# Optimization experiments

Hardware: AMD Instinct MI355X
Metric: run time of the kernel (lower is better)

## Reference

```python
import jax, jax.numpy as jnp
import numpy as np

# PlatonicConv (graph mode, attention=True, use_key=True): tetrahedron group G=12
G = 12
H_EFF = 2          # num_heads // G = 24 // 12
HEAD_D = 16        # embed_dim_g // H_EFF = (384//12) // 2
GH = G * H_EFF     # 24
IN_C = 384
EMB = 384
OUT_C = 384
N_GRAPHS = 32
NODES_PER_GRAPH = 64
N = N_GRAPHS * NODES_PER_GRAPH   # 2048
SPATIAL = 3


def _fc_edges():
    # fully-connected edges within each graph (batch[src]==batch[dst]), incl. self loops
    n = NODES_PER_GRAPH
    offs = np.arange(N_GRAPHS, dtype=np.int32) * n
    gs, gd = np.meshgrid(np.arange(n, dtype=np.int32), np.arange(n, dtype=np.int32), indexing='ij')
    src = (offs[:, None] + gs.reshape(-1)[None, :]).reshape(-1)
    dst = (offs[:, None] + gd.reshape(-1)[None, :]).reshape(-1)
    return jnp.asarray(src), jnp.asarray(dst)


def setup_inputs() -> dict:
    key = jax.random.key(0)
    ks = jax.random.split(key, 12)
    sw = 1.0 / np.sqrt(IN_C)
    x = jax.random.normal(ks[0], (N, IN_C), jnp.float32)
    pos = jax.random.normal(ks[1], (N, SPATIAL), jnp.float32)
    Wq = jax.random.normal(ks[2], (IN_C, EMB), jnp.float32) * sw
    bq = jnp.zeros((EMB,), jnp.float32)
    Wk = jax.random.normal(ks[3], (IN_C, EMB), jnp.float32) * sw
    bk = jnp.zeros((EMB,), jnp.float32)
    Wv = jax.random.normal(ks[4], (IN_C, EMB), jnp.float32) * sw
    bv = jnp.zeros((EMB,), jnp.float32)
    Wo = jax.random.normal(ks[5], (EMB, OUT_C), jnp.float32) * (1.0 / np.sqrt(EMB))
    bo = jnp.zeros((OUT_C,), jnp.float32)
    # RoPE frequencies: freq_sigma=1.0, random init, per spatial dim / head / half-dim
    rope_freqs = jax.random.normal(ks[6], (SPATIAL, H_EFF, HEAD_D // 2), jnp.float32)
    src, dst = _fc_edges()
    return {"x": x, "pos": pos, "Wq": Wq, "bq": bq, "Wk": Wk, "bk": bk,
            "Wv": Wv, "bv": bv, "Wo": Wo, "bo": bo, "rope_freqs": rope_freqs,
            "src": src, "dst": dst}


def _rope(t, pos, freqs):
    # t: [N, G, H, D]; pos: [N, 3]; freqs: [3, H, D//2]
    theta = jnp.einsum('ns,shf->nhf', pos, freqs)            # [N, H, D/2]
    cos = jnp.cos(theta)[:, None, :, :]                      # broadcast over G
    sin = jnp.sin(theta)[:, None, :, :]
    tr = t.reshape(t.shape[:-1] + (HEAD_D // 2, 2))
    t1, t2 = tr[..., 0], tr[..., 1]
    rot = jnp.stack([t1 * cos - t2 * sin, t1 * sin + t2 * cos], axis=-1)
    return rot.reshape(t.shape)


def reference(x, pos, Wq, bq, Wk, bk, Wv, bv, Wo, bo, rope_freqs, src, dst):
    n = x.shape[0]
    q = (x @ Wq + bq).reshape(n, G, H_EFF, HEAD_D)
    k = (x @ Wk + bk).reshape(n, G, H_EFF, HEAD_D)
    v = (x @ Wv + bv).reshape(n, G, H_EFF, HEAD_D)
    q = _rope(q, pos, rope_freqs)
    k = _rope(k, pos, rope_freqs)
    qf = q.reshape(n, GH, HEAD_D)
    kf = k.reshape(n, GH, HEAD_D)
    vf = v.reshape(n, GH, HEAD_D)
    # gather by edge index
    q_src = qf[src]                                          # [E, GH, D]
    k_dst = kf[dst]
    v_dst = vf[dst]
    scores = jnp.sum(q_src * k_dst, axis=-1) * (HEAD_D ** -0.5)  # [E, GH]
    # scatter softmax over edges grouped by src node (per group-head)
    m = jax.ops.segment_max(scores, src, num_segments=n)     # [N, GH]
    ex = jnp.exp(scores - m[src])
    den = jax.ops.segment_sum(ex, src, num_segments=n)
    a = ex / den[src]                                        # [E, GH]
    out = jax.ops.segment_sum(a[..., None] * v_dst, src, num_segments=n)  # [N, GH, D]
    out = out.reshape(n, GH * HEAD_D)
    return out @ Wo + bo
```

## Files before the change

kernel.cpp:

```cpp
#include <hip/hip_runtime.h>


#define NNODES   2048
#define KDIM     384
#define QKV_N    1152
#define NGRAPHS  32
#define NPG      64
#define GHEADS   24
#define HDIM     16

typedef __attribute__((ext_vector_type(8))) short short8;
typedef __attribute__((ext_vector_type(4))) float f32x4;

__device__ __forceinline__ short f2bf(float f) {
    unsigned u = __builtin_bit_cast(unsigned, f);
    u += 0x7FFFu + ((u >> 16) & 1u);
    return (short)(u >> 16);
}

__global__ __launch_bounds__(256) void prep_kernel(
    const float* __restrict__ x,
    const float* __restrict__ Wq, const float* __restrict__ Wk,
    const float* __restrict__ Wv, const float* __restrict__ Wo,
    const float* __restrict__ bq, const float* __restrict__ bk,
    const float* __restrict__ bv,
    short* __restrict__ WT, short* __restrict__ xb,
    float* __restrict__ bias_cat)
{
    const int b   = blockIdx.x;
    const int tid = threadIdx.x;
    if (b < 576) {
        __shared__ float tile[32][33];
        const int mat = b / 144;
        const int t   = b - mat * 144;
        const int k0  = (t / 12) * 32;
        const int n0  = (t % 12) * 32;
        const float* W = (mat == 0) ? Wq : (mat == 1) ? Wk : (mat == 2) ? Wv : Wo;
        const int cx = tid & 31;
        const int ty = tid >> 5;
        #pragma unroll
        for (int i = 0; i < 4; ++i) {
            const int rr = ty + 8 * i;
            tile[rr][cx] = W[(size_t)(k0 + rr) * KDIM + n0 + cx];
        }
        __syncthreads();
        #pragma unroll
        for (int i = 0; i < 4; ++i) {
            const int rr = ty + 8 * i;
            WT[(size_t)(mat * 384 + n0 + rr) * KDIM + k0 + cx] = f2bf(tile[cx][rr]);
        }
    } else if (b < 960) {
        const int idx = ((b - 576) * 256 + tid) * 8;
        const f32x4* xp = reinterpret_cast<const f32x4*>(x + idx);
        f32x4 v0 = xp[0], v1 = xp[1];
        short8 o;
        o[0] = f2bf(v0[0]); o[1] = f2bf(v0[1]); o[2] = f2bf(v0[2]); o[3] = f2bf(v0[3]);
        o[4] = f2bf(v1[0]); o[5] = f2bf(v1[1]); o[6] = f2bf(v1[2]); o[7] = f2bf(v1[3]);
        *reinterpret_cast<short8*>(xb + idx) = o;
    } else {
        for (int i = tid; i < QKV_N; i += 256) {
            const int seg = i / 384;
            const float* bp = (seg == 0) ? bq : (seg == 1) ? bk : bv;
            bias_cat[i] = bp[i - seg * 384];
        }
    }
}

__global__ __launch_bounds__(256) void gemm_kernel(
    const short* __restrict__ A,
    const short* __restrict__ BT,
    const float* __restrict__ bias,
    float* __restrict__ C, int ldc,
    const float* __restrict__ pos, const float* __restrict__ freqs,
    int do_rope)
{
    __shared__ __align__(16) short As[64 * 72];
    __shared__ __align__(16) short Bs[64 * 72];

    const int tid = threadIdx.x;
    const int m0  = blockIdx.x * 64;
    const int n0  = blockIdx.y * 64;

    const int r  = tid >> 2;
    const int kq = (tid & 3) * 16;

    const int lane = tid & 63;
    const int w    = tid >> 6;
    const int wr   = (w >> 1) * 32;
    const int wc   = (w & 1) * 32;
    const int fr   = lane & 15;
    const int ko   = (lane >> 4) * 8;

    const short* aRow = A  + (size_t)(m0 + r) * KDIM;
    const short* bRow = BT + (size_t)(n0 + r) * KDIM;

    short8 a0 = *reinterpret_cast<const short8*>(aRow + kq);
    short8 a1 = *reinterpret_cast<const short8*>(aRow + kq + 8);
    short8 b0 = *reinterpret_cast<const short8*>(bRow + kq);
    short8 b1 = *reinterpret_cast<const short8*>(bRow + kq + 8);
    *reinterpret_cast<short8*>(&As[r * 72 + kq])     = a0;
    *reinterpret_cast<short8*>(&As[r * 72 + kq + 8]) = a1;
    *reinterpret_cast<short8*>(&Bs[r * 72 + kq])     = b0;
    *reinterpret_cast<short8*>(&Bs[r * 72 + kq + 8]) = b1;
    __syncthreads();

    f32x4 acc[2][2];
    #pragma unroll
    for (int i = 0; i < 2; ++i)
        #pragma unroll
        for (int j = 0; j < 2; ++j)
            acc[i][j] = (f32x4){0.f, 0.f, 0.f, 0.f};

    for (int kt = 0;; kt += 64) {
        const bool has_next = (kt + 64) < KDIM;
        short8 na0, na1, nb0, nb1;
        if (has_next) {
            na0 = *reinterpret_cast<const short8*>(aRow + kt + 64 + kq);
            na1 = *reinterpret_cast<const short8*>(aRow + kt + 64 + kq + 8);
            nb0 = *reinterpret_cast<const short8*>(bRow + kt + 64 + kq);
            nb1 = *reinterpret_cast<const short8*>(bRow + kt + 64 + kq + 8);
        }
        #pragma unroll
        for (int kk = 0; kk < 64; kk += 32) {
            short8 af0 = *reinterpret_cast<const short8*>(&As[(wr + fr) * 72 + kk + ko]);
            short8 af1 = *reinterpret_cast<const short8*>(&As[(wr + 16 + fr) * 72 + kk + ko]);
            short8 bf0 = *reinterpret_cast<const short8*>(&Bs[(wc + fr) * 72 + kk + ko]);
            short8 bf1 = *reinterpret_cast<const short8*>(&Bs[(wc + 16 + fr) * 72 + kk + ko]);
            acc[0][0] = __builtin_amdgcn_mfma_f32_16x16x32_bf16(af0, bf0, acc[0][0], 0, 0, 0);
            acc[0][1] = __builtin_amdgcn_mfma_f32_16x16x32_bf16(af0, bf1, acc[0][1], 0, 0, 0);
            acc[1][0] = __builtin_amdgcn_mfma_f32_16x16x32_bf16(af1, bf0, acc[1][0], 0, 0, 0);
            acc[1][1] = __builtin_amdgcn_mfma_f32_16x16x32_bf16(af1, bf1, acc[1][1], 0, 0, 0);
        }
        if (!has_next) break;
        __syncthreads();
        *reinterpret_cast<short8*>(&As[r * 72 + kq])     = na0;
        *reinterpret_cast<short8*>(&As[r * 72 + kq + 8]) = na1;
        *reinterpret_cast<short8*>(&Bs[r * 72 + kq])     = nb0;
        *reinterpret_cast<short8*>(&Bs[r * 72 + kq + 8]) = nb1;
        __syncthreads();
    }

    const bool rope_wave = do_rope && (n0 < 768);
    #pragma unroll
    for (int ni = 0; ni < 2; ++ni) {
        const int c  = n0 + wc + ni * 16 + fr;
        const float bv = bias[c];
        float F0 = 0.f, F1 = 0.f, F2 = 0.f;
        if (rope_wave) {
            const int f = fr >> 1;
            const int h = (c >> 4) & 1;
            F0 = freqs[h * 8 + f];
            F1 = freqs[16 + h * 8 + f];
            F2 = freqs[32 + h * 8 + f];
        }
        #pragma unroll
        for (int mi = 0; mi < 2; ++mi) {
            const int rowb = m0 + wr + mi * 16 + (lane >> 4) * 4;
            float v[4];
            #pragma unroll
            for (int rr = 0; rr < 4; ++rr)
                v[rr] = acc[mi][ni][rr] + bv;
            if (rope_wave) {
                #pragma unroll
                for (int rr = 0; rr < 4; ++rr) {
                    const int row = rowb + rr;
                    const float th = pos[row * 3] * F0 + pos[row * 3 + 1] * F1
                                   + pos[row * 3 + 2] * F2;
                    const float cs = __cosf(th);
                    const float sn = __sinf(th);
                    const float other = __shfl_xor(v[rr], 1, 64);
                    v[rr] = (fr & 1) ? (other * sn + v[rr] * cs)
                                     : (v[rr] * cs - other * sn);
                }
            }
            #pragma unroll
            for (int rr = 0; rr < 4; ++rr)
                C[(size_t)(rowb + rr) * ldc + c] = v[rr];
        }
    }
}

__global__ __launch_bounds__(64) void attn_kernel(
    const float* __restrict__ qkv,
    short* __restrict__ attn_out)
{
    const int blk  = blockIdx.x;
    const int gr   = blk / GHEADS;
    const int gh   = blk - gr * GHEADS;
    const int lane = threadIdx.x;
    const int n    = gr * NPG + lane;

    const float* rowq = qkv + (size_t)n * QKV_N + gh * HDIM;

    __shared__ float klds[NPG][HDIM];
    __shared__ float vlds[NPG][HDIM];

    f32x4 q[4];
    #pragma unroll
    for (int i = 0; i < 4; ++i)
        q[i] = reinterpret_cast<const f32x4*>(rowq)[i];
    #pragma unroll
    for (int i = 0; i < 4; ++i)
        reinterpret_cast<f32x4*>(&klds[lane][0])[i] =
            reinterpret_cast<const f32x4*>(rowq + 384)[i];
    #pragma unroll
    for (int i = 0; i < 4; ++i)
        reinterpret_cast<f32x4*>(&vlds[lane][0])[i] =
            reinterpret_cast<const f32x4*>(rowq + 768)[i];
    __syncthreads();

    float sc[NPG];
    #pragma unroll
    for (int j = 0; j < NPG; ++j) {
        const f32x4* kp = reinterpret_cast<const f32x4*>(&klds[j][0]);
        f32x4 k0 = kp[0], k1 = kp[1], k2 = kp[2], k3 = kp[3];
        float a = q[0][0]*k0[0] + q[0][1]*k0[1] + q[0][2]*k0[2] + q[0][3]*k0[3]
                + q[1][0]*k1[0] + q[1][1]*k1[1] + q[1][2]*k1[2] + q[1][3]*k1[3]
                + q[2][0]*k2[0] + q[2][1]*k2[1] + q[2][2]*k2[2] + q[2][3]*k2[3]
                + q[3][0]*k3[0] + q[3][1]*k3[1] + q[3][2]*k3[2] + q[3][3]*k3[3];
        sc[j] = a * 0.25f;
    }

    float m = sc[0];
    #pragma unroll
    for (int j = 1; j < NPG; ++j) m = fmaxf(m, sc[j]);

    float den = 0.f;
    #pragma unroll
    for (int j = 0; j < NPG; ++j) {
        sc[j] = __expf(sc[j] - m);
        den += sc[j];
    }

    float o[HDIM];
    #pragma unroll
    for (int d = 0; d < HDIM; ++d) o[d] = 0.f;
    #pragma unroll
    for (int j = 0; j < NPG; ++j) {
        const float p = sc[j];
        const f32x4* vp = reinterpret_cast<const f32x4*>(&vlds[j][0]);
        f32x4 v0 = vp[0], v1 = vp[1], v2 = vp[2], v3 = vp[3];
        #pragma unroll
        for (int d = 0; d < 4; ++d) {
            o[d]      += p * v0[d];
            o[4 + d]  += p * v1[d];
            o[8 + d]  += p * v2[d];
            o[12 + d] += p * v3[d];
        }
    }

    const float inv = 1.0f / den;
    short8 r0, r1;
    #pragma unroll
    for (int d = 0; d < 8; ++d) {
        r0[d] = f2bf(o[d] * inv);
        r1[d] = f2bf(o[8 + d] * inv);
    }
    short* outp = attn_out + (size_t)n * 384 + gh * HDIM;
    *reinterpret_cast<short8*>(outp)     = r0;
    *reinterpret_cast<short8*>(outp + 8) = r1;
}

extern "C" void kernel_launch(void* const* d_in, const int* in_sizes, int n_in,
                              void* d_out, int out_size, void* d_ws, size_t ws_size,
                              hipStream_t stream) {
    const float* x    = (const float*)d_in[0];
    const float* pos  = (const float*)d_in[1];
    const float* Wq   = (const float*)d_in[2];
    const float* bq   = (const float*)d_in[3];
    const float* Wk   = (const float*)d_in[4];
    const float* bk   = (const float*)d_in[5];
    const float* Wv   = (const float*)d_in[6];
    const float* bv   = (const float*)d_in[7];
    const float* Wo   = (const float*)d_in[8];
    const float* bo   = (const float*)d_in[9];
    const float* rope = (const float*)d_in[10];

    char* ws = (char*)d_ws;
    short* WT       = (short*)(ws);
    short* xb       = (short*)(ws + 1179648);
    float* bias_cat = (float*)(ws + 2752512);
    float* qkv      = (float*)(ws + 2757120);
    short* attn     = (short*)(ws + 12194304);

    prep_kernel<<<961, 256, 0, stream>>>(x, Wq, Wk, Wv, Wo, bq, bk, bv,
                                         WT, xb, bias_cat);

    {
        dim3 grid(NNODES / 64, QKV_N / 64);
        gemm_kernel<<<grid, 256, 0, stream>>>(xb, WT, bias_cat, qkv, QKV_N,
                                              pos, rope, 1);
    }

    attn_kernel<<<NGRAPHS * GHEADS, 64, 0, stream>>>(qkv, attn);

    {
        dim3 grid(NNODES / 64, KDIM / 64);
        gemm_kernel<<<grid, 256, 0, stream>>>(attn, WT + (size_t)1152 * KDIM, bo,
                                              (float*)d_out, KDIM, pos, rope, 0);
    }
}
```

Before: 109.8 us.

## Fuse QKV projection with per-graph attention and shrink output GEMM tiles

Each attention block (one graph, one group-head) now computes its own Q, K, V slices with MFMA straight from global bf16 data, applies bias and RoPE, and runs softmax-attention with four waves that split the keys and combine results with cross-lane shuffles. This removes the fp32 QKV round trip through global memory and one kernel launch. The output GEMM becomes a one-wave 16x64 tile kernel with no LDS staging, which gives many more blocks. The trade-off is that tiles are no longer shared through LDS, so the x and weight rows are reloaded from global or L2 by each block.

New measurement: 113.8 us. 1.04x slower.

```diff
diff --git a/kernel.cpp b/kernel.cpp
--- a/kernel.cpp
+++ b/kernel.cpp
@@ -3,7 +3,6 @@
 
 #define NNODES   2048
 #define KDIM     384
-#define QKV_N    1152
 #define NGRAPHS  32
 #define NPG      64
 #define GHEADS   24
@@ -22,10 +21,7 @@
     const float* __restrict__ x,
     const float* __restrict__ Wq, const float* __restrict__ Wk,
     const float* __restrict__ Wv, const float* __restrict__ Wo,
-    const float* __restrict__ bq, const float* __restrict__ bk,
-    const float* __restrict__ bv,
-    short* __restrict__ WT, short* __restrict__ xb,
-    float* __restrict__ bias_cat)
+    short* __restrict__ WT, short* __restrict__ xb)
 {
     const int b   = blockIdx.x;
     const int tid = threadIdx.x;
@@ -49,7 +45,7 @@
             const int rr = ty + 8 * i;
             WT[(size_t)(mat * 384 + n0 + rr) * KDIM + k0 + cx] = f2bf(tile[cx][rr]);
         }
-    } else if (b < 960) {
+    } else {
         const int idx = ((b - 576) * 256 + tid) * 8;
         const f32x4* xp = reinterpret_cast<const f32x4*>(x + idx);
         f32x4 v0 = xp[0], v1 = xp[1];
@@ -57,189 +53,128 @@
         o[0] = f2bf(v0[0]); o[1] = f2bf(v0[1]); o[2] = f2bf(v0[2]); o[3] = f2bf(v0[3]);
         o[4] = f2bf(v1[0]); o[5] = f2bf(v1[1]); o[6] = f2bf(v1[2]); o[7] = f2bf(v1[3]);
         *reinterpret_cast<short8*>(xb + idx) = o;
-    } else {
-        for (int i = tid; i < QKV_N; i += 256) {
-            const int seg = i / 384;
-            const float* bp = (seg == 0) ? bq : (seg == 1) ? bk : bv;
-            bias_cat[i] = bp[i - seg * 384];
-        }
-    }
-}
-
-__global__ __launch_bounds__(256) void gemm_kernel(
-    const short* __restrict__ A,
-    const short* __restrict__ BT,
-    const float* __restrict__ bias,
-    float* __restrict__ C, int ldc,
+    }
+}
+
+__global__ __launch_bounds__(256) void qkv_attn_kernel(
+    const short* __restrict__ xb,
+    const short* __restrict__ WT,
+    const float* __restrict__ bq, const float* __restrict__ bk,
+    const float* __restrict__ bv,
     const float* __restrict__ pos, const float* __restrict__ freqs,
-    int do_rope)
-{
-    __shared__ __align__(16) short As[64 * 72];
-    __shared__ __align__(16) short Bs[64 * 72];
-
-    const int tid = threadIdx.x;
-    const int m0  = blockIdx.x * 64;
-    const int n0  = blockIdx.y * 64;
-
-    const int r  = tid >> 2;
-    const int kq = (tid & 3) * 16;
-
-    const int lane = tid & 63;
-    const int w    = tid >> 6;
-    const int wr   = (w >> 1) * 32;
-    const int wc   = (w & 1) * 32;
-    const int fr   = lane & 15;
-    const int ko   = (lane >> 4) * 8;
-
-    const short* aRow = A  + (size_t)(m0 + r) * KDIM;
-    const short* bRow = BT + (size_t)(n0 + r) * KDIM;
-
-    short8 a0 = *reinterpret_cast<const short8*>(aRow + kq);
-    short8 a1 = *reinterpret_cast<const short8*>(aRow + kq + 8);
-    short8 b0 = *reinterpret_cast<const short8*>(bRow + kq);
-    short8 b1 = *reinterpret_cast<const short8*>(bRow + kq + 8);
-    *reinterpret_cast<short8*>(&As[r * 72 + kq])     = a0;
-    *reinterpret_cast<short8*>(&As[r * 72 + kq + 8]) = a1;
-    *reinterpret_cast<short8*>(&Bs[r * 72 + kq])     = b0;
-    *reinterpret_cast<short8*>(&Bs[r * 72 + kq + 8]) = b1;
-    __syncthreads();
-
-    f32x4 acc[2][2];
-    #pragma unroll
-    for (int i = 0; i < 2; ++i)
-        #pragma unroll
-        for (int j = 0; j < 2; ++j)
-            acc[i][j] = (f32x4){0.f, 0.f, 0.f, 0.f};
-
-    for (int kt = 0;; kt += 64) {
-        const bool has_next = (kt + 64) < KDIM;
-        short8 na0, na1, nb0, nb1;
-        if (has_next) {
-            na0 = *reinterpret_cast<const short8*>(aRow + kt + 64 + kq);
-            na1 = *reinterpret_cast<const short8*>(aRow + kt + 64 + kq + 8);
-            nb0 = *reinterpret_cast<const short8*>(bRow + kt + 64 + kq);
-            nb1 = *reinterpret_cast<const short8*>(bRow + kt + 64 + kq + 8);
-        }
-        #pragma unroll
-        for (int kk = 0; kk < 64; kk += 32) {
-            short8 af0 = *reinterpret_cast<const short8*>(&As[(wr + fr) * 72 + kk + ko]);
-            short8 af1 = *reinterpret_cast<const short8*>(&As[(wr + 16 + fr) * 72 + kk + ko]);
-            short8 bf0 = *reinterpret_cast<const short8*>(&Bs[(wc + fr) * 72 + kk + ko]);
-            short8 bf1 = *reinterpret_cast<const short8*>(&Bs[(wc + 16 + fr) * 72 + kk + ko]);
-            acc[0][0] = __builtin_amdgcn_mfma_f32_16x16x32_bf16(af0, bf0, acc[0][0], 0, 0, 0);
-            acc[0][1] = __builtin_amdgcn_mfma_f32_16x16x32_bf16(af0, bf1, acc[0][1], 0, 0, 0);
-            acc[1][0] = __builtin_amdgcn_mfma_f32_16x16x32_bf16(af1, bf0, acc[1][0], 0, 0, 0);
-            acc[1][1] = __builtin_amdgcn_mfma_f32_16x16x32_bf16(af1, bf1, acc[1][1], 0, 0, 0);
-        }
-        if (!has_next) break;
-        __syncthreads();
-        *reinterpret_cast<short8*>(&As[r * 72 + kq])     = na0;
-        *reinterpret_cast<short8*>(&As[r * 72 + kq + 8]) = na1;
-        *reinterpret_cast<short8*>(&Bs[r * 72 + kq])     = nb0;
-        *reinterpret_cast<short8*>(&Bs[r * 72 + kq + 8]) = nb1;
-        __syncthreads();
-    }
-
-    const bool rope_wave = do_rope && (n0 < 768);
-    #pragma unroll
-    for (int ni = 0; ni < 2; ++ni) {
-        const int c  = n0 + wc + ni * 16 + fr;
-        const float bv = bias[c];
-        float F0 = 0.f, F1 = 0.f, F2 = 0.f;
-        if (rope_wave) {
-            const int f = fr >> 1;
-            const int h = (c >> 4) & 1;
-            F0 = freqs[h * 8 + f];
-            F1 = freqs[16 + h * 8 + f];
-            F2 = freqs[32 + h * 8 + f];
-        }
-        #pragma unroll
-        for (int mi = 0; mi < 2; ++mi) {
-            const int rowb = m0 + wr + mi * 16 + (lane >> 4) * 4;
-            float v[4];
-            #pragma unroll
-            for (int rr = 0; rr < 4; ++rr)
-                v[rr] = acc[mi][ni][rr] + bv;
-            if (rope_wave) {
-                #pragma unroll
-                for (int rr = 0; rr < 4; ++rr) {
-                    const int row = rowb + rr;
-                    const float th = pos[row * 3] * F0 + pos[row * 3 + 1] * F1
-                                   + pos[row * 3 + 2] * F2;
-                    const float cs = __cosf(th);
-                    const float sn = __sinf(th);
-                    const float other = __shfl_xor(v[rr], 1, 64);
-                    v[rr] = (fr & 1) ? (other * sn + v[rr] * cs)
-                                     : (v[rr] * cs - other * sn);
-                }
-            }
-            #pragma unroll
-            for (int rr = 0; rr < 4; ++rr)
-                C[(size_t)(rowb + rr) * ldc + c] = v[rr];
-        }
-    }
-}
-
-__global__ __launch_bounds__(64) void attn_kernel(
-    const float* __restrict__ qkv,
     short* __restrict__ attn_out)
 {
     const int blk  = blockIdx.x;
     const int gr   = blk / GHEADS;
     const int gh   = blk - gr * GHEADS;
-    const int lane = threadIdx.x;
-    const int n    = gr * NPG + lane;
-
-    const float* rowq = qkv + (size_t)n * QKV_N + gh * HDIM;
-
-    __shared__ float klds[NPG][HDIM];
-    __shared__ float vlds[NPG][HDIM];
-
-    f32x4 q[4];
-    #pragma unroll
-    for (int i = 0; i < 4; ++i)
-        q[i] = reinterpret_cast<const f32x4*>(rowq)[i];
-    #pragma unroll
-    for (int i = 0; i < 4; ++i)
-        reinterpret_cast<f32x4*>(&klds[lane][0])[i] =
-            reinterpret_cast<const f32x4*>(rowq + 384)[i];
-    #pragma unroll
-    for (int i = 0; i < 4; ++i)
-        reinterpret_cast<f32x4*>(&vlds[lane][0])[i] =
-            reinterpret_cast<const f32x4*>(rowq + 768)[i];
+    const int tid  = threadIdx.x;
+    const int w    = tid >> 6;
+    const int lane = tid & 63;
+    const int fr   = lane & 15;
+    const int hi   = lane >> 4;
+
+    const short* aP  = xb + (size_t)(gr * 64 + w * 16 + fr) * KDIM + hi * 8;
+    const short* bqP = WT + (size_t)(gh * 16 + fr) * KDIM + hi * 8;
+    const short* bkP = bqP + (size_t)384 * KDIM;
+    const short* bvP = bkP + (size_t)384 * KDIM;
+
+    f32x4 acc[3];
+    acc[0] = (f32x4){0.f, 0.f, 0.f, 0.f};
+    acc[1] = acc[0];
+    acc[2] = acc[0];
+
+    #pragma unroll 4
+    for (int kt = 0; kt < KDIM; kt += 32) {
+        short8 af = *reinterpret_cast<const short8*>(aP + kt);
+        short8 b0 = *reinterpret_cast<const short8*>(bqP + kt);
+        short8 b1 = *reinterpret_cast<const short8*>(bkP + kt);
+        short8 b2 = *reinterpret_cast<const short8*>(bvP + kt);
+        acc[0] = __builtin_amdgcn_mfma_f32_16x16x32_bf16(af, b0, acc[0], 0, 0, 0);
+        acc[1] = __builtin_amdgcn_mfma_f32_16x16x32_bf16(af, b1, acc[1], 0, 0, 0);
+        acc[2] = __builtin_amdgcn_mfma_f32_16x16x32_bf16(af, b2, acc[2], 0, 0, 0);
+    }
+
+    __shared__ float q_lds[64][20];
+    __shared__ float k_lds[64][20];
+    __shared__ float v_lds[64][20];
+
+    const float bias_q = bq[gh * 16 + fr];
+    const float bias_k = bk[gh * 16 + fr];
+    const float bias_v = bv[gh * 16 + fr];
+    const int   h = gh & 1;
+    const int   f = fr >> 1;
+    const float F0 = freqs[h * 8 + f];
+    const float F1 = freqs[16 + h * 8 + f];
+    const float F2 = freqs[32 + h * 8 + f];
+
+    #pragma unroll
+    for (int rr = 0; rr < 4; ++rr) {
+        const int row  = w * 16 + hi * 4 + rr;
+        const int grow = gr * 64 + row;
+        float qv = acc[0][rr] + bias_q;
+        float kv = acc[1][rr] + bias_k;
+        float vv = acc[2][rr] + bias_v;
+        const float th = pos[grow * 3] * F0 + pos[grow * 3 + 1] * F1
+                       + pos[grow * 3 + 2] * F2;
+        const float cs = __cosf(th);
+        const float sn = __sinf(th);
+        const float qo = __shfl_xor(qv, 1, 64);
+        const float ko = __shfl_xor(kv, 1, 64);
+        qv = (fr & 1) ? (qo * sn + qv * cs) : (qv * cs - qo * sn);
+        kv = (fr & 1) ? (ko * sn + kv * cs) : (kv * cs - ko * sn);
+        q_lds[row][fr] = qv;
+        k_lds[row][fr] = kv;
+        v_lds[row][fr] = vv;
+    }
     __syncthreads();
 
-    float sc[NPG];
-    #pragma unroll
-    for (int j = 0; j < NPG; ++j) {
-        const f32x4* kp = reinterpret_cast<const f32x4*>(&klds[j][0]);
-        f32x4 k0 = kp[0], k1 = kp[1], k2 = kp[2], k3 = kp[3];
-        float a = q[0][0]*k0[0] + q[0][1]*k0[1] + q[0][2]*k0[2] + q[0][3]*k0[3]
-                + q[1][0]*k1[0] + q[1][1]*k1[1] + q[1][2]*k1[2] + q[1][3]*k1[3]
-                + q[2][0]*k2[0] + q[2][1]*k2[1] + q[2][2]*k2[2] + q[2][3]*k2[3]
-                + q[3][0]*k3[0] + q[3][1]*k3[1] + q[3][2]*k3[2] + q[3][3]*k3[3];
+    const int qrow = w * 16 + fr;
+    f32x4 q0 = *reinterpret_cast<const f32x4*>(&q_lds[qrow][0]);
+    f32x4 q1 = *reinterpret_cast<const f32x4*>(&q_lds[qrow][4]);
+    f32x4 q2 = *reinterpret_cast<const f32x4*>(&q_lds[qrow][8]);
+    f32x4 q3 = *reinterpret_cast<const f32x4*>(&q_lds[qrow][12]);
+
+    float sc[16];
+    #pragma unroll
+    for (int j = 0; j < 16; ++j) {
+        const float* kp = &k_lds[hi * 16 + j][0];
+        f32x4 k0 = reinterpret_cast<const f32x4*>(kp)[0];
+        f32x4 k1 = reinterpret_cast<const f32x4*>(kp)[1];
+        f32x4 k2 = reinterpret_cast<const f32x4*>(kp)[2];
+        f32x4 k3 = reinterpret_cast<const f32x4*>(kp)[3];
+        float a = q0[0]*k0[0] + q0[1]*k0[1] + q0[2]*k0[2] + q0[3]*k0[3]
+                + q1[0]*k1[0] + q1[1]*k1[1] + q1[2]*k1[2] + q1[3]*k1[3]
+                + q2[0]*k2[0] + q2[1]*k2[1] + q2[2]*k2[2] + q2[3]*k2[3]
+                + q3[0]*k3[0] + q3[1]*k3[1] + q3[2]*k3[2] + q3[3]*k3[3];
         sc[j] = a * 0.25f;
     }
 
-    float m = sc[0];
-    #pragma unroll
-    for (int j = 1; j < NPG; ++j) m = fmaxf(m, sc[j]);
+    float mx = sc[0];
+    #pragma unroll
+    for (int j = 1; j < 16; ++j) mx = fmaxf(mx, sc[j]);
+    mx = fmaxf(mx, __shfl_xor(mx, 16, 64));
+    mx = fmaxf(mx, __shfl_xor(mx, 32, 64));
 
     float den = 0.f;
     #pragma unroll
-    for (int j = 0; j < NPG; ++j) {
-        sc[j] = __expf(sc[j] - m);
+    for (int j = 0; j < 16; ++j) {
+        sc[j] = __expf(sc[j] - mx);
         den += sc[j];
     }
-
-    float o[HDIM];
-    #pragma unroll
-    for (int d = 0; d < HDIM; ++d) o[d] = 0.f;
-    #pragma unroll
-    for (int j = 0; j < NPG; ++j) {
+    den += __shfl_xor(den, 16, 64);
+    den += __shfl_xor(den, 32, 64);
+
+    float o[16];
+    #pragma unroll
+    for (int d = 0; d < 16; ++d) o[d] = 0.f;
+    #pragma unroll
+    for (int j = 0; j < 16; ++j) {
         const float p = sc[j];
-        const f32x4* vp = reinterpret_cast<const f32x4*>(&vlds[j][0]);
-        f32x4 v0 = vp[0], v1 = vp[1], v2 = vp[2], v3 = vp[3];
+        const float* vp = &v_lds[hi * 16 + j][0];
+        f32x4 v0 = reinterpret_cast<const f32x4*>(vp)[0];
+        f32x4 v1 = reinterpret_cast<const f32x4*>(vp)[1];
+        f32x4 v2 = reinterpret_cast<const f32x4*>(vp)[2];
+        f32x4 v3 = reinterpret_cast<const f32x4*>(vp)[3];
         #pragma unroll
         for (int d = 0; d < 4; ++d) {
             o[d]      += p * v0[d];
@@ -248,17 +183,70 @@
             o[12 + d] += p * v3[d];
         }
     }
-
-    const float inv = 1.0f / den;
-    short8 r0, r1;
-    #pragma unroll
-    for (int d = 0; d < 8; ++d) {
-        r0[d] = f2bf(o[d] * inv);
-        r1[d] = f2bf(o[8 + d] * inv);
-    }
-    short* outp = attn_out + (size_t)n * 384 + gh * HDIM;
-    *reinterpret_cast<short8*>(outp)     = r0;
-    *reinterpret_cast<short8*>(outp + 8) = r1;
+    #pragma unroll
+    for (int d = 0; d < 16; ++d) {
+        o[d] += __shfl_xor(o[d], 16, 64);
+        o[d] += __shfl_xor(o[d], 32, 64);
+    }
+
+    if (hi == 0) {
+        const float inv = 1.0f / den;
+        short8 r0, r1;
+        #pragma unroll
+        for (int d = 0; d < 8; ++d) {
+            r0[d] = f2bf(o[d] * inv);
+            r1[d] = f2bf(o[8 + d] * inv);
+        }
+        short* op = attn_out + (size_t)(gr * 64 + qrow) * KDIM + gh * 16;
+        *reinterpret_cast<short8*>(op)     = r0;
+        *reinterpret_cast<short8*>(op + 8) = r1;
+    }
+}
+
+__global__ __launch_bounds__(64) void out_gemm_kernel(
+    const short* __restrict__ A,
+    const short* __restrict__ BT,
+    const float* __restrict__ bias,
+    float* __restrict__ C)
+{
+    const int r0   = blockIdx.x * 16;
+    const int c0   = blockIdx.y * 64;
+    const int lane = threadIdx.x;
+    const int fr   = lane & 15;
+    const int hi   = lane >> 4;
+
+    const short* aP = A + (size_t)(r0 + fr) * KDIM + hi * 8;
+    const short* b0P = BT + (size_t)(c0 + fr) * KDIM + hi * 8;
+    const short* b1P = b0P + (size_t)16 * KDIM;
+    const short* b2P = b1P + (size_t)16 * KDIM;
+    const short* b3P = b2P + (size_t)16 * KDIM;
+
+    f32x4 acc[4];
+    acc[0] = (f32x4){0.f, 0.f, 0.f, 0.f};
+    acc[1] = acc[0]; acc[2] = acc[0]; acc[3] = acc[0];
+
+    #pragma unroll 4
+    for (int kt = 0; kt < KDIM; kt += 32) {
+        short8 af = *reinterpret_cast<const short8*>(aP + kt);
+        short8 f0 = *reinterpret_cast<const short8*>(b0P + kt);
+        short8 f1 = *reinterpret_cast<const short8*>(b1P + kt);
+        short8 f2 = *reinterpret_cast<const short8*>(b2P + kt);
+        short8 f3 = *reinterpret_cast<const short8*>(b3P + kt);
+        acc[0] = __builtin_amdgcn_mfma_f32_16x16x32_bf16(af, f0, acc[0], 0, 0, 0);
+        acc[1] = __builtin_amdgcn_mfma_f32_16x16x32_bf16(af, f1, acc[1], 0, 0, 0);
+        acc[2] = __builtin_amdgcn_mfma_f32_16x16x32_bf16(af, f2, acc[2], 0, 0, 0);
+        acc[3] = __builtin_amdgcn_mfma_f32_16x16x32_bf16(af, f3, acc[3], 0, 0, 0);
+    }
+
+    #pragma unroll
+    for (int ct = 0; ct < 4; ++ct) {
+        const int c  = c0 + ct * 16 + fr;
+        const float bv = bias[c];
+        const int rowb = r0 + hi * 4;
+        #pragma unroll
+        for (int rr = 0; rr < 4; ++rr)
+            C[(size_t)(rowb + rr) * KDIM + c] = acc[ct][rr] + bv;
+    }
 }
 
 extern "C" void kernel_launch(void* const* d_in, const int* in_sizes, int n_in,
@@ -277,26 +265,18 @@
     const float* rope = (const float*)d_in[10];
 
     char* ws = (char*)d_ws;
-    short* WT       = (short*)(ws);
-    short* xb       = (short*)(ws + 1179648);
-    float* bias_cat = (float*)(ws + 2752512);
-    float* qkv      = (float*)(ws + 2757120);
-    short* attn     = (short*)(ws + 12194304);
-
-    prep_kernel<<<961, 256, 0, stream>>>(x, Wq, Wk, Wv, Wo, bq, bk, bv,
-                                         WT, xb, bias_cat);
+    short* WT   = (short*)(ws);
+    short* xb   = (short*)(ws + 1179648);
+    short* attn = (short*)(ws + 2752512);
+
+    prep_kernel<<<960, 256, 0, stream>>>(x, Wq, Wk, Wv, Wo, WT, xb);
+
+    qkv_attn_kernel<<<NGRAPHS * GHEADS, 256, 0, stream>>>(
+        xb, WT, bq, bk, bv, pos, rope, attn);
 
     {
-        dim3 grid(NNODES / 64, QKV_N / 64);
-        gemm_kernel<<<grid, 256, 0, stream>>>(xb, WT, bias_cat, qkv, QKV_N,
-                                              pos, rope, 1);
-    }
-
-    attn_kernel<<<NGRAPHS * GHEADS, 64, 0, stream>>>(qkv, attn);
-
-    {
-        dim3 grid(NNODES / 64, KDIM / 64);
-        gemm_kernel<<<grid, 256, 0, stream>>>(attn, WT + (size_t)1152 * KDIM, bo,
-                                              (float*)d_out, KDIM, pos, rope, 0);
-    }
-}
+        dim3 grid(NNODES / 16, KDIM / 64);
+        out_gemm_kernel<<<grid, 64, 0, stream>>>(
+            attn, WT + (size_t)1152 * KDIM, bo, (float*)d_out);
+    }
+}
```
